# Kernel optimization log

Hardware: AMD Instinct MI355X
Metric: run time of the kernel (lower is better)

Reference implementation:

```python
import jax, jax.numpy as jnp
import numpy as np

D_MODEL = 1024
NUM_HEAD = 16
D_HEAD = D_MODEL // NUM_HEAD


def setup_inputs() -> dict:
    key = jax.random.key(0)
    kx, kq, kk, kv, ko = jax.random.split(key, 5)
    x = jax.random.normal(kx, (2, 2048, D_MODEL), dtype=jnp.float32)
    p_q = jax.random.normal(kq, (D_MODEL, D_MODEL), dtype=jnp.float32)
    p_k = jax.random.normal(kk, (D_MODEL, D_MODEL), dtype=jnp.float32)
    p_v = jax.random.normal(kv, (D_MODEL, D_MODEL), dtype=jnp.float32)
    p_o = jax.random.normal(ko, (D_MODEL, D_MODEL), dtype=jnp.float32)
    return {"x": x, "p_q": p_q, "p_k": p_k, "p_v": p_v, "p_o": p_o}


def reference(x, p_q, p_k, p_v, p_o):
    B, S, _ = x.shape
    # project: weight viewed as [H, d_head, d_model]; out[b,h,s,d] = sum_m x[b,s,m] W[h,d,m]
    wq = p_q.reshape(NUM_HEAD, D_HEAD, D_MODEL)
    wk = p_k.reshape(NUM_HEAD, D_HEAD, D_MODEL)
    wv = p_v.reshape(NUM_HEAD, D_HEAD, D_MODEL)
    q = jnp.einsum('bsm,hdm->bhsd', x, wq)
    k = jnp.einsum('bsm,hdm->bhsd', x, wk)
    v = jnp.einsum('bsm,hdm->bhsd', x, wv)
    # full causal attention, scores scaled by 1/sqrt(d_head)
    scores = jnp.einsum('bhqd,bhkd->bhqk', q, k) / jnp.sqrt(jnp.float32(D_HEAD))
    causal = jnp.tril(jnp.ones((S, S), dtype=bool))
    scores = jnp.where(causal, scores, -jnp.inf)
    attn = jax.nn.softmax(scores, axis=-1)
    out = jnp.einsum('bhqk,bhkd->bhqd', attn, v)
    out = out.transpose(0, 2, 1, 3).reshape(B, S, D_MODEL)  # [B,S,H*d_head]
    # output proj: einsum '... d1, d2 d1 -> ... d2' == out @ p_o.T
    return jnp.einsum('bsm,nm->bsn', out, p_o)
```

## Files before the change

kernel.cpp:

```cpp
#include <hip/hip_runtime.h>
#include <stdint.h>

#define D_MODEL 1024
#define SEQ     2048
#define NHEAD   16
#define BATCH   2
#define NROWS   (BATCH*SEQ)

typedef _Float16 f16;
typedef _Float16 f16x8 __attribute__((ext_vector_type(8)));
typedef _Float16 f16x4 __attribute__((ext_vector_type(4)));
typedef __fp16   h16x2 __attribute__((ext_vector_type(2)));
typedef float    f32x4 __attribute__((ext_vector_type(4)));

#define MFMA16 __builtin_amdgcn_mfma_f32_16x16x32_f16

__device__ __forceinline__ void gload16(const void* g, void* l) {
  __builtin_amdgcn_global_load_lds(
      (const __attribute__((address_space(1))) void*)g,
      (__attribute__((address_space(3))) void*)l, 16, 0, 0);
}

__device__ __forceinline__ int pkh2(float a, float b) {
  union { h16x2 h; int i; } u;
  u.h = __builtin_amdgcn_cvt_pkrtz(a, b);
  return u.i;
}

__global__ void split4_kernel(const float* __restrict__ in, f16* __restrict__ hi,
                              f16* __restrict__ lo, int n4, float scale) {
  int i = blockIdx.x * blockDim.x + threadIdx.x;
  if (i >= n4) return;
  float4 v = reinterpret_cast<const float4*>(in)[i];
  v.x *= scale; v.y *= scale; v.z *= scale; v.w *= scale;
  f16x4 h, l4;
  h[0] = (f16)v.x; h[1] = (f16)v.y; h[2] = (f16)v.z; h[3] = (f16)v.w;
  l4[0] = (f16)(v.x - (float)h[0]);
  l4[1] = (f16)(v.y - (float)h[1]);
  l4[2] = (f16)(v.z - (float)h[2]);
  l4[3] = (f16)(v.w - (float)h[3]);
  *reinterpret_cast<f16x4*>(hi + 4*(size_t)i) = h;
  *reinterpret_cast<f16x4*>(lo + 4*(size_t)i) = l4;
}

__global__ void prep_w_kernel(const float* __restrict__ pq, const float* __restrict__ pk,
                              const float* __restrict__ pv, const float* __restrict__ po,
                              f16* __restrict__ wq_hi, f16* __restrict__ wq_lo,
                              f16* __restrict__ wk_hi, f16* __restrict__ wk_lo,
                              f16* __restrict__ wv_h,  f16* __restrict__ wo_h,
                              int n4, float qscale) {
  int i = blockIdx.x * blockDim.x + threadIdx.x;
  if (i >= n4) return;
  {
    float4 v = reinterpret_cast<const float4*>(pq)[i];
    v.x *= qscale; v.y *= qscale; v.z *= qscale; v.w *= qscale;
    f16x4 h, l4;
    h[0] = (f16)v.x; h[1] = (f16)v.y; h[2] = (f16)v.z; h[3] = (f16)v.w;
    l4[0] = (f16)(v.x - (float)h[0]); l4[1] = (f16)(v.y - (float)h[1]);
    l4[2] = (f16)(v.z - (float)h[2]); l4[3] = (f16)(v.w - (float)h[3]);
    *reinterpret_cast<f16x4*>(wq_hi + 4*(size_t)i) = h;
    *reinterpret_cast<f16x4*>(wq_lo + 4*(size_t)i) = l4;
  }
  {
    float4 v = reinterpret_cast<const float4*>(pk)[i];
    f16x4 h, l4;
    h[0] = (f16)v.x; h[1] = (f16)v.y; h[2] = (f16)v.z; h[3] = (f16)v.w;
    l4[0] = (f16)(v.x - (float)h[0]); l4[1] = (f16)(v.y - (float)h[1]);
    l4[2] = (f16)(v.z - (float)h[2]); l4[3] = (f16)(v.w - (float)h[3]);
    *reinterpret_cast<f16x4*>(wk_hi + 4*(size_t)i) = h;
    *reinterpret_cast<f16x4*>(wk_lo + 4*(size_t)i) = l4;
  }
  {
    float4 v = reinterpret_cast<const float4*>(pv)[i];
    f16x4 h;
    h[0] = (f16)v.x; h[1] = (f16)v.y; h[2] = (f16)v.z; h[3] = (f16)v.w;
    *reinterpret_cast<f16x4*>(wv_h + 4*(size_t)i) = h;
  }
  {
    float4 v = reinterpret_cast<const float4*>(po)[i];
    f16x4 h;
    h[0] = (f16)v.x; h[1] = (f16)v.y; h[2] = (f16)v.z; h[3] = (f16)v.w;
    *reinterpret_cast<f16x4*>(wo_h + 4*(size_t)i) = h;
  }
}

template<bool SPLIT_IN, bool SPLIT_OUT, bool F32_OUT, bool COLCHUNK>
__global__ __launch_bounds__(256, 2)
void gemm_nt(const f16* __restrict__ Ahi, const f16* __restrict__ Alo,
             const f16* __restrict__ Bhi, const f16* __restrict__ Blo,
             f16* __restrict__ Chi, f16* __restrict__ Clo, float* __restrict__ Cf,
             int M, int N, int K)
{
  constexpr int ALO_OFF = 8192;
  constexpr int B_OFF   = SPLIT_IN ? 16384 : 8192;
  constexpr int BLO_OFF = 20480;
  constexpr int STRIDE  = SPLIT_IN ? 24576 : 12288;
  __shared__ __align__(16) char smem[2 * STRIDE];

  const int tid = threadIdx.x;
  const int w = tid >> 6, l = tid & 63;
  const int wr = (w >> 1) * 64;
  const int wc = (w & 1) * 32;

  const int gx = gridDim.x, gy = gridDim.y;
  const int nwg = gx * gy;
  const int flat = blockIdx.y * gx + blockIdx.x;
  const int swz = (flat & 7) * (nwg >> 3) + (flat >> 3);
  const int bxn = COLCHUNK ? (swz / gy) : (swz % gx);
  const int byn = COLCHUNK ? (swz % gy) : (swz / gx);
  const int bm = byn * 128, bn = bxn * 64;

  f32x4 acc[4][2] = {};

  const int srow = tid >> 2;
  const int schunk = 8 * (((tid & 3) ^ ((srow >> 1) & 3)));

  auto stage = [&](int kt) {
    char* dst = smem + (kt & 1) * STRIDE;
    const int k0 = kt * 32;
    const f16* ga = Ahi + (size_t)(bm + srow) * K + k0 + schunk;
    gload16(ga,        dst + (w << 10));
    gload16(ga + 64*K, dst + 4096 + (w << 10));
    const f16* gb = Bhi + (size_t)(bn + srow) * K + k0 + schunk;
    gload16(gb,        dst + B_OFF + (w << 10));
    if (SPLIT_IN) {
      const f16* gal = Alo + (size_t)(bm + srow) * K + k0 + schunk;
      gload16(gal,        dst + ALO_OFF + (w << 10));
      gload16(gal + 64*K, dst + ALO_OFF + 4096 + (w << 10));
      const f16* gbl = Blo + (size_t)(bn + srow) * K + k0 + schunk;
      gload16(gbl,        dst + BLO_OFF + (w << 10));
    }
  };

  const int nkt = K >> 5;
  stage(0);

  for (int kt = 0; kt < nkt; kt++) {
    if (kt + 1 < nkt) {
      stage(kt + 1);
      if constexpr (SPLIT_IN) asm volatile("s_waitcnt vmcnt(6)" ::: "memory");
      else                    asm volatile("s_waitcnt vmcnt(3)" ::: "memory");
    } else {
      asm volatile("s_waitcnt vmcnt(0)" ::: "memory");
    }
    __builtin_amdgcn_s_barrier();

    const char* buf = smem + (kt & 1) * STRIDE;
    const int ar = (l & 15);
    const int ak = 16 * ((l >> 4) ^ ((ar >> 1) & 3));
    f16x8 a_hi[4], a_lo[4];
#pragma unroll
    for (int mi = 0; mi < 4; mi++) {
      a_hi[mi] = *(const f16x8*)(buf + (size_t)(wr + mi*16 + ar) * 64 + ak);
      if (SPLIT_IN)
        a_lo[mi] = *(const f16x8*)(buf + ALO_OFF + (size_t)(wr + mi*16 + ar) * 64 + ak);
    }
    __builtin_amdgcn_s_setprio(1);
#pragma unroll
    for (int ni = 0; ni < 2; ni++) {
      f16x8 b_hi = *(const f16x8*)(buf + B_OFF + (size_t)(wc + ni*16 + ar) * 64 + ak);
      f16x8 b_lo = {};
      if (SPLIT_IN)
        b_lo = *(const f16x8*)(buf + BLO_OFF + (size_t)(wc + ni*16 + ar) * 64 + ak);
#pragma unroll
      for (int mi = 0; mi < 4; mi++) {
        acc[mi][ni] = MFMA16(a_hi[mi], b_hi, acc[mi][ni], 0, 0, 0);
        if (SPLIT_IN) {
          acc[mi][ni] = MFMA16(a_hi[mi], b_lo, acc[mi][ni], 0, 0, 0);
          acc[mi][ni] = MFMA16(a_lo[mi], b_hi, acc[mi][ni], 0, 0, 0);
        }
      }
    }
    __builtin_amdgcn_s_setprio(0);
    __builtin_amdgcn_s_barrier();
  }

  const int crow0 = bm + wr + (l >> 4) * 4;
  const int ccol0 = bn + wc + (l & 15);
#pragma unroll
  for (int mi = 0; mi < 4; mi++) {
#pragma unroll
    for (int ni = 0; ni < 2; ni++) {
#pragma unroll
      for (int j = 0; j < 4; j++) {
        size_t idx = (size_t)(crow0 + mi*16 + j) * N + (ccol0 + ni*16);
        float v = acc[mi][ni][j];
        if (F32_OUT) {
          Cf[idx] = v;
        } else {
          f16 h = (f16)v;
          Chi[idx] = h;
          if (SPLIT_OUT) Clo[idx] = (f16)(v - (float)h);
        }
      }
    }
  }
}

__global__ __launch_bounds__(512, 4)
void attn_kernel(const f16* __restrict__ Qhi, const f16* __restrict__ Qlo,
                 const f16* __restrict__ Khi, const f16* __restrict__ Klo,
                 const f16* __restrict__ VT, f16* __restrict__ Out)
{
  __shared__ __align__(16) char smem[49152];

  const int tid = threadIdx.x, w = tid >> 6, l = tid & 63;
  const int g = l >> 4, q4 = l & 15;
  const int wi = w & 3, grp = w >> 2;
  const int flat = blockIdx.x;
  const int xcd = flat & 7, slot = flat >> 3;
  const int bh = xcd * 4 + (slot >> 4);
  const int c = slot & 15;
  const int b = bh >> 4, h = bh & 15;
  const int bS = b * SEQ;
  const size_t hoff = (size_t)h * 64;
  const int T  = 64 - 2 * c;
  const int P1 = 2 * c + 2;
  const int P2 = 31 - 2 * c;

  int qw = (grp ? (31 - c) : c) * 64 + wi * 16;

  f16x8 qh[2], ql[2];
  auto loadQ = [&]() {
#pragma unroll
    for (int ks = 0; ks < 2; ks++) {
      const size_t base = (size_t)(bS + qw + q4) * D_MODEL + hoff + ks * 32 + g * 8;
      qh[ks] = *(const f16x8*)(Qhi + base);
      ql[ks] = *(const f16x8*)(Qlo + base);
    }
  };
  loadQ();

  f32x4 o[4] = {};
  float m_run = -INFINITY, l_run = 0.f;

  const int k_src = 8 * ((l & 7) ^ (l >> 3));
  const int v_src = 8 * ((l & 3) ^ ((l >> 2) & 3));

  auto stage = [&](int t) {
    const int kv0 = t * 32;
    char* sb = smem + (t & 3) * 12288;
    if (w < 4) {
      const f16* src = (w < 2) ? Khi : Klo;
      char* dstc = sb + ((w < 2) ? 0 : 4096);
      const int wi2 = w & 1;
#pragma unroll
      for (int gi = 0; gi < 2; gi++) {
        const int sub = 2 * wi2 + gi;
        const int row = 8 * sub + (l >> 3);
        gload16(src + (size_t)(bS + kv0 + row) * D_MODEL + hoff + k_src,
                dstc + sub * 1024);
      }
    } else if (w < 6) {
      const int wi2 = w - 4;
#pragma unroll
      for (int gi = 0; gi < 2; gi++) {
        const int sub = 2 * wi2 + gi;
        const int drow = 16 * sub + (l >> 2);
        gload16(VT + (hoff + drow) * (size_t)NROWS + bS + kv0 + v_src,
                sb + 8192 + sub * 1024);
      }
    }
  };

  const int idx_lo = (q4 + 32 * (g & 1)) * 4;
  const int idx_hi = idx_lo + 64;
  const bool upper = (l >= 32);

  auto compute = [&](int t) {
    const char* sb = smem + (t & 3) * 12288;
    const int kv0 = t * 32;

    f32x4 s[2] = {};
    __builtin_amdgcn_s_setprio(1);
#pragma unroll
    for (int ni = 0; ni < 2; ni++) {
      const int row = ni * 16 + q4;
#pragma unroll
      for (int ks = 0; ks < 2; ks++) {
        const int boff = row * 128 + 16 * ((ks * 4 + g) ^ (row & 7));
        f16x8 kh8 = *(const f16x8*)(sb + boff);
        f16x8 kl8 = *(const f16x8*)(sb + 4096 + boff);
        s[ni] = MFMA16(kh8, qh[ks], s[ni], 0, 0, 0);
        s[ni] = MFMA16(kh8, ql[ks], s[ni], 0, 0, 0);
        s[ni] = MFMA16(kl8, qh[ks], s[ni], 0, 0, 0);
      }
    }
    __builtin_amdgcn_s_setprio(0);

    const bool need_mask = (kv0 + 31) > qw;
    const int q_abs = qw + q4;
    float p[2][4];
    float pm = -INFINITY;
#pragma unroll
    for (int ni = 0; ni < 2; ni++)
#pragma unroll
      for (int j = 0; j < 4; j++) {
        float v = s[ni][j];
        if (need_mask && (kv0 + ni * 16 + 4 * g + j) > q_abs) v = -INFINITY;
        p[ni][j] = v;
        pm = fmaxf(pm, v);
      }
    pm = fmaxf(pm, __shfl_xor(pm, 16));
    pm = fmaxf(pm, __shfl_xor(pm, 32));

    if (!__all(pm - m_run <= 8.0f)) {
      const float mn = fmaxf(m_run, pm);
      const float sc = __builtin_amdgcn_exp2f(m_run - mn);
      m_run = mn;
      l_run *= sc;
#pragma unroll
      for (int nd = 0; nd < 4; nd++)
#pragma unroll
        for (int j = 0; j < 4; j++) o[nd][j] *= sc;
    }
    float ps = 0.f;
#pragma unroll
    for (int ni = 0; ni < 2; ni++)
#pragma unroll
      for (int j = 0; j < 4; j++) {
        const float e = __builtin_amdgcn_exp2f(p[ni][j] - m_run);
        p[ni][j] = e;
        ps += e;
      }
    ps += __shfl_xor(ps, 16);
    ps += __shfl_xor(ps, 32);
    l_run += ps;

    const int pk0 = pkh2(p[0][0], p[0][1]);
    const int pk1 = pkh2(p[0][2], p[0][3]);
    const int pk2 = pkh2(p[1][0], p[1][1]);
    const int pk3 = pkh2(p[1][2], p[1][3]);
    const int b0l = __builtin_amdgcn_ds_bpermute(idx_lo, pk0);
    const int b2l = __builtin_amdgcn_ds_bpermute(idx_lo, pk2);
    const int b1l = __builtin_amdgcn_ds_bpermute(idx_lo, pk1);
    const int b3l = __builtin_amdgcn_ds_bpermute(idx_lo, pk3);
    const int b0h = __builtin_amdgcn_ds_bpermute(idx_hi, pk0);
    const int b2h = __builtin_amdgcn_ds_bpermute(idx_hi, pk2);
    const int b1h = __builtin_amdgcn_ds_bpermute(idx_hi, pk1);
    const int b3h = __builtin_amdgcn_ds_bpermute(idx_hi, pk3);
    union { int u[4]; f16x8 v; } pu;
    pu.u[0] = upper ? b2l : b0l;
    pu.u[1] = upper ? b3l : b1l;
    pu.u[2] = upper ? b2h : b0h;
    pu.u[3] = upper ? b3h : b1h;
    const f16x8 pa = pu.v;

    __builtin_amdgcn_s_setprio(1);
#pragma unroll
    for (int nd = 0; nd < 4; nd++) {
      const int d = nd * 16 + q4;
      f16x8 bv = *(const f16x8*)(sb + 8192 + d * 64 + 16 * (g ^ (d & 3)));
      o[nd] = MFMA16(bv, pa, o[nd], 0, 0, 0);
    }
    __builtin_amdgcn_s_setprio(0);
  };

  stage(0);
  stage(1);

  for (int t = 0; t < P1; t++) {
    stage(t + 2);
    asm volatile("s_waitcnt vmcnt(4)" ::: "memory");
    __builtin_amdgcn_s_barrier();
    compute(t);
    __builtin_amdgcn_s_barrier();
  }

  if (grp == 0) {
    const float inv = 1.0f / l_run;
    const size_t rowb = (size_t)(bS + qw + q4) * D_MODEL + hoff;
#pragma unroll
    for (int nd = 0; nd < 4; nd++) {
      f16x4 v;
#pragma unroll
      for (int j = 0; j < 4; j++) v[j] = (f16)(o[nd][j] * inv);
      *reinterpret_cast<f16x4*>(Out + rowb + nd * 16 + 4 * g) = v;
    }
    qw = (31 - c) * 64 + wi * 16;
    loadQ();
#pragma unroll
    for (int nd = 0; nd < 4; nd++)
#pragma unroll
      for (int j = 0; j < 4; j++) o[nd][j] = 0.f;
    m_run = -INFINITY;
    l_run = 0.f;
  }

  for (int j = 0; j < P2; j++) {
    const int u = P1 + 2 * j;
    const bool st = (u + 3) < T;
    if (st) { stage(u + 2); stage(u + 3); }
    if (st) asm volatile("s_waitcnt vmcnt(4)" ::: "memory");
    else    asm volatile("s_waitcnt vmcnt(0)" ::: "memory");
    __builtin_amdgcn_s_barrier();
    compute(u + grp);
    __builtin_amdgcn_s_barrier();
  }

  if (grp == 0) {
    float* mb = (float*)smem + wi * 1152 + l * 18;
#pragma unroll
    for (int nd = 0; nd < 4; nd++)
#pragma unroll
      for (int j = 0; j < 4; j++) mb[nd * 4 + j] = o[nd][j];
    mb[16] = m_run;
    mb[17] = l_run;
  }
  __syncthreads();
  if (grp == 1) {
    const float* mb = (const float*)smem + wi * 1152 + l * 18;
    const float m2 = mb[16], l2 = mb[17];
    const float mm = fmaxf(m_run, m2);
    const float a1 = __builtin_amdgcn_exp2f(m_run - mm);
    const float a2 = __builtin_amdgcn_exp2f(m2 - mm);
    const float inv = 1.0f / (l_run * a1 + l2 * a2);
    const size_t rowb = (size_t)(bS + qw + q4) * D_MODEL + hoff;
#pragma unroll
    for (int nd = 0; nd < 4; nd++) {
      f16x4 v;
#pragma unroll
      for (int j = 0; j < 4; j++)
        v[j] = (f16)((o[nd][j] * a1 + mb[nd * 4 + j] * a2) * inv);
      *reinterpret_cast<f16x4*>(Out + rowb + nd * 16 + 4 * g) = v;
    }
  }
}

extern "C" void kernel_launch(void* const* d_in, const int* in_sizes, int n_in,
                              void* d_out, int out_size, void* d_ws, size_t ws_size,
                              hipStream_t stream) {
  const float* x  = (const float*)d_in[0];
  const float* pq = (const float*)d_in[1];
  const float* pk = (const float*)d_in[2];
  const float* pv = (const float*)d_in[3];
  const float* po = (const float*)d_in[4];
  float* out = (float*)d_out;

  char* ws = (char*)d_ws;
  size_t off = 0;
  auto alloc = [&](size_t elems) {
    f16* p = (f16*)(ws + off);
    off += ((elems * 2 + 255) & ~(size_t)255);
    return p;
  };
  f16* x_hi  = alloc((size_t)NROWS * D_MODEL);
  f16* x_lo  = alloc((size_t)NROWS * D_MODEL);
  f16* wq_hi = alloc((size_t)D_MODEL * D_MODEL);
  f16* wq_lo = alloc((size_t)D_MODEL * D_MODEL);
  f16* wk_hi = alloc((size_t)D_MODEL * D_MODEL);
  f16* wk_lo = alloc((size_t)D_MODEL * D_MODEL);
  f16* wv_h  = alloc((size_t)D_MODEL * D_MODEL);
  f16* wo_h  = alloc((size_t)D_MODEL * D_MODEL);
  f16* q_hi  = alloc((size_t)NROWS * D_MODEL);
  f16* q_lo  = alloc((size_t)NROWS * D_MODEL);
  f16* k_hi  = alloc((size_t)NROWS * D_MODEL);
  f16* k_lo  = alloc((size_t)NROWS * D_MODEL);
  f16* vt    = alloc((size_t)NROWS * D_MODEL);
  f16* ao    = alloc((size_t)NROWS * D_MODEL);

  const int n4x = NROWS * D_MODEL / 4;
  const int n4w = D_MODEL * D_MODEL / 4;
  const float qscale = 0.125f * 1.44269504088896f;
  split4_kernel<<<n4x/256, 256, 0, stream>>>(x, x_hi, x_lo, n4x, 1.0f);
  prep_w_kernel<<<n4w/256, 256, 0, stream>>>(pq, pk, pv, po,
                                             wq_hi, wq_lo, wk_hi, wk_lo, wv_h, wo_h,
                                             n4w, qscale);

  dim3 gg(D_MODEL/64, NROWS/128);
  gemm_nt<true,  true,  false, false><<<gg, 256, 0, stream>>>(x_hi, x_lo, wq_hi, wq_lo, q_hi, q_lo, nullptr, NROWS, D_MODEL, D_MODEL);
  gemm_nt<true,  true,  false, false><<<gg, 256, 0, stream>>>(x_hi, x_lo, wk_hi, wk_lo, k_hi, k_lo, nullptr, NROWS, D_MODEL, D_MODEL);
  dim3 gv(NROWS/64, D_MODEL/128);
  gemm_nt<false, false, false, true><<<gv, 256, 0, stream>>>(wv_h, nullptr, x_hi, nullptr, vt, nullptr, nullptr, D_MODEL, NROWS, D_MODEL);

  attn_kernel<<<dim3(512), 512, 0, stream>>>(q_hi, q_lo, k_hi, k_lo, vt, ao);

  gemm_nt<false, false, true, false><<<gg, 256, 0, stream>>>(ao, nullptr, wo_h, nullptr, nullptr, nullptr, out, NROWS, D_MODEL, D_MODEL);
}
```

Measured before the change: 180.3 us.

## Fuse Q and K split-precision projections into one GEMM sharing X tiles

```diff
diff --git a/kernel.cpp b/kernel.cpp
--- a/kernel.cpp
+++ b/kernel.cpp
@@ -84,17 +84,15 @@
   }
 }
 
-template<bool SPLIT_IN, bool SPLIT_OUT, bool F32_OUT, bool COLCHUNK>
+template<bool F32_OUT, bool COLCHUNK>
 __global__ __launch_bounds__(256, 2)
-void gemm_nt(const f16* __restrict__ Ahi, const f16* __restrict__ Alo,
-             const f16* __restrict__ Bhi, const f16* __restrict__ Blo,
-             f16* __restrict__ Chi, f16* __restrict__ Clo, float* __restrict__ Cf,
+void gemm_nt(const f16* __restrict__ Ahi,
+             const f16* __restrict__ Bhi,
+             f16* __restrict__ Chi, float* __restrict__ Cf,
              int M, int N, int K)
 {
-  constexpr int ALO_OFF = 8192;
-  constexpr int B_OFF   = SPLIT_IN ? 16384 : 8192;
-  constexpr int BLO_OFF = 20480;
-  constexpr int STRIDE  = SPLIT_IN ? 24576 : 12288;
+  constexpr int B_OFF  = 8192;
+  constexpr int STRIDE = 12288;
   __shared__ __align__(16) char smem[2 * STRIDE];
 
   const int tid = threadIdx.x;
@@ -123,13 +121,6 @@
     gload16(ga + 64*K, dst + 4096 + (w << 10));
     const f16* gb = Bhi + (size_t)(bn + srow) * K + k0 + schunk;
     gload16(gb,        dst + B_OFF + (w << 10));
-    if (SPLIT_IN) {
-      const f16* gal = Alo + (size_t)(bm + srow) * K + k0 + schunk;
-      gload16(gal,        dst + ALO_OFF + (w << 10));
-      gload16(gal + 64*K, dst + ALO_OFF + 4096 + (w << 10));
-      const f16* gbl = Blo + (size_t)(bn + srow) * K + k0 + schunk;
-      gload16(gbl,        dst + BLO_OFF + (w << 10));
-    }
   };
 
   const int nkt = K >> 5;
@@ -138,8 +129,96 @@
   for (int kt = 0; kt < nkt; kt++) {
     if (kt + 1 < nkt) {
       stage(kt + 1);
-      if constexpr (SPLIT_IN) asm volatile("s_waitcnt vmcnt(6)" ::: "memory");
-      else                    asm volatile("s_waitcnt vmcnt(3)" ::: "memory");
+      asm volatile("s_waitcnt vmcnt(3)" ::: "memory");
+    } else {
+      asm volatile("s_waitcnt vmcnt(0)" ::: "memory");
+    }
+    __builtin_amdgcn_s_barrier();
+
+    const char* buf = smem + (kt & 1) * STRIDE;
+    const int ar = (l & 15);
+    const int ak = 16 * ((l >> 4) ^ ((ar >> 1) & 3));
+    f16x8 a_hi[4];
+#pragma unroll
+    for (int mi = 0; mi < 4; mi++)
+      a_hi[mi] = *(const f16x8*)(buf + (size_t)(wr + mi*16 + ar) * 64 + ak);
+    __builtin_amdgcn_s_setprio(1);
+#pragma unroll
+    for (int ni = 0; ni < 2; ni++) {
+      f16x8 b_hi = *(const f16x8*)(buf + B_OFF + (size_t)(wc + ni*16 + ar) * 64 + ak);
+#pragma unroll
+      for (int mi = 0; mi < 4; mi++)
+        acc[mi][ni] = MFMA16(a_hi[mi], b_hi, acc[mi][ni], 0, 0, 0);
+    }
+    __builtin_amdgcn_s_setprio(0);
+    __builtin_amdgcn_s_barrier();
+  }
+
+  const int crow0 = bm + wr + (l >> 4) * 4;
+  const int ccol0 = bn + wc + (l & 15);
+#pragma unroll
+  for (int mi = 0; mi < 4; mi++) {
+#pragma unroll
+    for (int ni = 0; ni < 2; ni++) {
+#pragma unroll
+      for (int j = 0; j < 4; j++) {
+        size_t idx = (size_t)(crow0 + mi*16 + j) * N + (ccol0 + ni*16);
+        float v = acc[mi][ni][j];
+        if (F32_OUT) Cf[idx] = v;
+        else         Chi[idx] = (f16)v;
+      }
+    }
+  }
+}
+
+__global__ __launch_bounds__(256, 2)
+void gemm_qk(const f16* __restrict__ Ahi, const f16* __restrict__ Alo,
+             const f16* __restrict__ Bqh, const f16* __restrict__ Bql,
+             const f16* __restrict__ Bkh, const f16* __restrict__ Bkl,
+             f16* __restrict__ Qh, f16* __restrict__ Qlo2,
+             f16* __restrict__ Kh, f16* __restrict__ Klo2)
+{
+  constexpr int N = D_MODEL, K = D_MODEL;
+  constexpr int STRIDE = 32768;
+  __shared__ __align__(16) char smem[2 * STRIDE];
+
+  const int tid = threadIdx.x;
+  const int w = tid >> 6, l = tid & 63;
+  const int wr = (w >> 1) * 64;
+  const int wc = (w & 1) * 32;
+
+  const int flat = blockIdx.y * 16 + blockIdx.x;
+  const int swz = (flat & 7) * 64 + (flat >> 3);
+  const int bm = (swz / 16) * 128, bn = (swz % 16) * 64;
+
+  f32x4 accQ[4][2] = {}, accK[4][2] = {};
+
+  const int srow = tid >> 2;
+  const int schunk = 8 * (((tid & 3) ^ ((srow >> 1) & 3)));
+
+  auto stage = [&](int kt) {
+    char* dst = smem + (kt & 1) * STRIDE;
+    const int k0 = kt * 32;
+    const f16* ga = Ahi + (size_t)(bm + srow) * K + k0 + schunk;
+    gload16(ga,        dst + (w << 10));
+    gload16(ga + 64*K, dst + 4096 + (w << 10));
+    const f16* gal = Alo + (size_t)(bm + srow) * K + k0 + schunk;
+    gload16(gal,        dst + 8192 + (w << 10));
+    gload16(gal + 64*K, dst + 12288 + (w << 10));
+    const size_t bo = (size_t)(bn + srow) * K + k0 + schunk;
+    gload16(Bqh + bo, dst + 16384 + (w << 10));
+    gload16(Bql + bo, dst + 20480 + (w << 10));
+    gload16(Bkh + bo, dst + 24576 + (w << 10));
+    gload16(Bkl + bo, dst + 28672 + (w << 10));
+  };
+
+  const int nkt = K >> 5;
+  stage(0);
+
+  for (int kt = 0; kt < nkt; kt++) {
+    if (kt + 1 < nkt) {
+      stage(kt + 1);
+      asm volatile("s_waitcnt vmcnt(8)" ::: "memory");
     } else {
       asm volatile("s_waitcnt vmcnt(0)" ::: "memory");
     }
@@ -152,23 +231,24 @@
 #pragma unroll
     for (int mi = 0; mi < 4; mi++) {
       a_hi[mi] = *(const f16x8*)(buf + (size_t)(wr + mi*16 + ar) * 64 + ak);
-      if (SPLIT_IN)
-        a_lo[mi] = *(const f16x8*)(buf + ALO_OFF + (size_t)(wr + mi*16 + ar) * 64 + ak);
+      a_lo[mi] = *(const f16x8*)(buf + 8192 + (size_t)(wr + mi*16 + ar) * 64 + ak);
     }
     __builtin_amdgcn_s_setprio(1);
 #pragma unroll
     for (int ni = 0; ni < 2; ni++) {
-      f16x8 b_hi = *(const f16x8*)(buf + B_OFF + (size_t)(wc + ni*16 + ar) * 64 + ak);
-      f16x8 b_lo = {};
-      if (SPLIT_IN)
-        b_lo = *(const f16x8*)(buf + BLO_OFF + (size_t)(wc + ni*16 + ar) * 64 + ak);
+      const int bo = (wc + ni*16 + ar) * 64 + ak;
+      f16x8 bqh = *(const f16x8*)(buf + 16384 + bo);
+      f16x8 bql = *(const f16x8*)(buf + 20480 + bo);
+      f16x8 bkh = *(const f16x8*)(buf + 24576 + bo);
+      f16x8 bkl = *(const f16x8*)(buf + 28672 + bo);
 #pragma unroll
       for (int mi = 0; mi < 4; mi++) {
-        acc[mi][ni] = MFMA16(a_hi[mi], b_hi, acc[mi][ni], 0, 0, 0);
-        if (SPLIT_IN) {
-          acc[mi][ni] = MFMA16(a_hi[mi], b_lo, acc[mi][ni], 0, 0, 0);
-          acc[mi][ni] = MFMA16(a_lo[mi], b_hi, acc[mi][ni], 0, 0, 0);
-        }
+        accQ[mi][ni] = MFMA16(a_hi[mi], bqh, accQ[mi][ni], 0, 0, 0);
+        accQ[mi][ni] = MFMA16(a_hi[mi], bql, accQ[mi][ni], 0, 0, 0);
+        accQ[mi][ni] = MFMA16(a_lo[mi], bqh, accQ[mi][ni], 0, 0, 0);
+        accK[mi][ni] = MFMA16(a_hi[mi], bkh, accK[mi][ni], 0, 0, 0);
+        accK[mi][ni] = MFMA16(a_hi[mi], bkl, accK[mi][ni], 0, 0, 0);
+        accK[mi][ni] = MFMA16(a_lo[mi], bkh, accK[mi][ni], 0, 0, 0);
       }
     }
     __builtin_amdgcn_s_setprio(0);
@@ -184,14 +264,12 @@
 #pragma unroll
       for (int j = 0; j < 4; j++) {
         size_t idx = (size_t)(crow0 + mi*16 + j) * N + (ccol0 + ni*16);
-        float v = acc[mi][ni][j];
-        if (F32_OUT) {
-          Cf[idx] = v;
-        } else {
-          f16 h = (f16)v;
-          Chi[idx] = h;
-          if (SPLIT_OUT) Clo[idx] = (f16)(v - (float)h);
-        }
+        float qv = accQ[mi][ni][j];
+        f16 qh = (f16)qv;
+        Qh[idx] = qh;  Qlo2[idx] = (f16)(qv - (float)qh);
+        float kv = accK[mi][ni][j];
+        f16 kh = (f16)kv;
+        Kh[idx] = kh;  Klo2[idx] = (f16)(kv - (float)kh);
       }
     }
   }
@@ -467,13 +545,13 @@
                                              wq_hi, wq_lo, wk_hi, wk_lo, wv_h, wo_h,
                                              n4w, qscale);
 
+  gemm_qk<<<dim3(16, 32), 256, 0, stream>>>(x_hi, x_lo, wq_hi, wq_lo, wk_hi, wk_lo,
+                                            q_hi, q_lo, k_hi, k_lo);
+  dim3 gv(NROWS/64, D_MODEL/128);
+  gemm_nt<false, true><<<gv, 256, 0, stream>>>(wv_h, x_hi, vt, nullptr, D_MODEL, NROWS, D_MODEL);
+
+  attn_kernel<<<dim3(512), 512, 0, stream>>>(q_hi, q_lo, k_hi, k_lo, vt, ao);
+
   dim3 gg(D_MODEL/64, NROWS/128);
-  gemm_nt<true,  true,  false, false><<<gg, 256, 0, stream>>>(x_hi, x_lo, wq_hi, wq_lo, q_hi, q_lo, nullptr, NROWS, D_MODEL, D_MODEL);
-  gemm_nt<true,  true,  false, false><<<gg, 256, 0, stream>>>(x_hi, x_lo, wk_hi, wk_lo, k_hi, k_lo, nullptr, NROWS, D_MODEL, D_MODEL);
-  dim3 gv(NROWS/64, D_MODEL/128);
-  gemm_nt<false, false, false, true><<<gv, 256, 0, stream>>>(wv_h, nullptr, x_hi, nullptr, vt, nullptr, nullptr, D_MODEL, NROWS, D_MODEL);
-
-  attn_kernel<<<dim3(512), 512, 0, stream>>>(q_hi, q_lo, k_hi, k_lo, vt, ao);
-
-  gemm_nt<false, false, true, false><<<gg, 256, 0, stream>>>(ao, nullptr, wo_h, nullptr, nullptr, nullptr, out, NROWS, D_MODEL, D_MODEL);
-}
+  gemm_nt<true, false><<<gg, 256, 0, stream>>>(ao, wo_h, nullptr, out, NROWS, D_MODEL, D_MODEL);
+}
```

Result: faster. 166.2 us (-7.8%).
